# Optimization experiments

Measured on AMD Instinct MI355X. Metric: run time of the kernel, lower is better.

Reference implementation:

```python
import jax, jax.numpy as jnp
import numpy as np


def gcn_conv(x, W, b, src, dst):
    """PyG-style GCNConv: linear transform, then D^{-1/2}(A+I)D^{-1/2} aggregation."""
    N = x.shape[0]
    h = x @ W  # [N, out]
    # degree with self-loops: in-degree at target + 1
    deg = jax.ops.segment_sum(jnp.ones(src.shape[0], h.dtype), dst, num_segments=N) + 1.0
    dinv = jax.lax.rsqrt(deg)  # deg >= 1, always finite
    norm = dinv[src] * dinv[dst]  # [E]
    agg = jax.ops.segment_sum(h[src] * norm[:, None], dst, num_segments=N)
    # self-loop contribution: norm_ii = dinv_i^2
    agg = agg + h * (dinv * dinv)[:, None]
    return agg + b


def setup_inputs() -> dict:
    key = jax.random.key(0)
    ks = jax.random.split(key, 5)
    N, E, D = 50000, 800000, 512
    x = jax.random.normal(ks[0], (N, D), dtype=jnp.float32)
    edge_index = jax.random.randint(ks[1], (2, E), 0, N, dtype=jnp.int64)
    def glorot(k, fan_in, fan_out):
        s = jnp.sqrt(6.0 / (fan_in + fan_out)).astype(jnp.float32)
        return jax.random.uniform(k, (fan_in, fan_out), jnp.float32, -s, s)
    return {
        "x": x,
        "edge_index": edge_index,
        "W1": glorot(ks[2], 512, 128), "b1": jnp.zeros((128,), jnp.float32),
        "W2": glorot(ks[3], 128, 64), "b2": jnp.zeros((64,), jnp.float32),
        "W3": glorot(ks[4], 64, 64), "b3": jnp.zeros((64,), jnp.float32),
    }


def reference(x, edge_index, W1, b1, W2, b2, W3, b3):
    src, dst = edge_index[0], edge_index[1]
    h = gcn_conv(x, W1, b1, src, dst)
    h = jax.nn.leaky_relu(h, negative_slope=0.2)
    # dropout p=0.3 is identity in eval mode
    h = gcn_conv(h, W2, b2, src, dst)
    h = jax.nn.leaky_relu(h, negative_slope=0.2)
    h = gcn_conv(h, W3, b3, src, dst)
    return h
```

## Files before the change

kernel.cpp:

```cpp
#include <hip/hip_runtime.h>
#include <hip/hip_fp16.h>


typedef __attribute__((ext_vector_type(8))) short bf16x8;
typedef __attribute__((ext_vector_type(8))) _Float16 f16x8;
typedef __attribute__((ext_vector_type(4))) float f32x4;
typedef unsigned short u16;
typedef unsigned int u32;

static inline size_t alignup(size_t v, size_t a) { return (v + a - 1) & ~(a - 1); }

__device__ __forceinline__ u32 pack_hi16(u32 b0, u32 b1) {
    return __builtin_amdgcn_perm(b1, b0, 0x07060302u);
}

__device__ __forceinline__ void splitW_bf16(const float* __restrict__ W,
                                            u16* __restrict__ Wh,
                                            u16* __restrict__ Wl, int s, int F) {
    int c = s % F;
    int kb = (s / F) * 8;
    union { u32 u[4]; bf16x8 v; } hi, lo;
#pragma unroll
    for (int p = 0; p < 4; p++) {
        float x0 = W[(size_t)(kb + 2 * p) * F + c];
        float x1 = W[(size_t)(kb + 2 * p + 1) * F + c];
        u32 b0 = __float_as_uint(x0), b1 = __float_as_uint(x1);
        float l0 = x0 - __uint_as_float(b0 & 0xFFFF0000u);
        float l1 = x1 - __uint_as_float(b1 & 0xFFFF0000u);
        hi.u[p] = pack_hi16(b0, b1);
        lo.u[p] = pack_hi16(__float_as_uint(l0), __float_as_uint(l1));
    }
    *(bf16x8*)(Wh + (size_t)s * 8) = hi.v;
    *(bf16x8*)(Wl + (size_t)s * 8) = lo.v;
}

__device__ __forceinline__ void splitW_f16(const float* __restrict__ W,
                                           u16* __restrict__ Wh,
                                           u16* __restrict__ Wl, int s, int F) {
    int c = s % F;
    int kb = (s / F) * 8;
    union { u16 u[8]; bf16x8 v; } hi, lo;
#pragma unroll
    for (int p = 0; p < 8; p++) {
        float xv = W[(size_t)(kb + p) * F + c];
        __half h = __float2half(xv);
        __half l = __float2half(xv - __half2float(h));
        hi.u[p] = __half_as_ushort(h);
        lo.u[p] = __half_as_ushort(l);
    }
    *(bf16x8*)(Wh + (size_t)s * 8) = hi.v;
    *(bf16x8*)(Wl + (size_t)s * 8) = lo.v;
}

__global__ void k_init_deg(const int* __restrict__ ei, int E,
                           int* __restrict__ flag,
                           int* __restrict__ deg, int* __restrict__ rank,
                           const float* __restrict__ W1, u16* w1h, u16* w1l,
                           const float* __restrict__ W2, u16* w2h, u16* w2l,
                           const float* __restrict__ W3, u16* w3h, u16* w3l) {
    constexpr int SPLITB = 38;
    int b = blockIdx.x;
    if (b < SPLITB) {
        if (b == 0 && threadIdx.x < 64) {
            int v = ei[2 * threadIdx.x + 1];
            unsigned long long m = __ballot(v != 0);
            if (threadIdx.x == 0) *flag = (m == 0ull) ? 1 : 0;
        }
        int s = b * 256 + threadIdx.x;
        if (s < 8192) splitW_bf16(W1, w1h, w1l, s, 128);
        else if (s < 9216) splitW_f16(W2, w2h, w2l, s - 8192, 64);
        else if (s < 9728) splitW_f16(W3, w3h, w3l, s - 9216, 64);
        return;
    }
    int v = ei[2 * (threadIdx.x & 63) + 1];
    unsigned long long m = __ballot(v != 0);
    int is64 = (m == 0ull) ? 1 : 0;
    int i = (b - SPLITB) * 256 + threadIdx.x;
    if (i >= E) return;
    int d = is64 ? ei[2 * (E + i)] : ei[E + i];
    rank[i] = atomicAdd(&deg[d], 1);
}

__global__ void k_scan1(const int* __restrict__ deg, int* __restrict__ offs,
                        int* __restrict__ bsums, float* __restrict__ dinv, int N) {
    __shared__ int s[256];
    int i = blockIdx.x * 256 + threadIdx.x;
    int v = (i < N) ? deg[i] : 0;
    if (i < N) dinv[i] = rsqrtf((float)v + 1.0f);
    s[threadIdx.x] = v;
    __syncthreads();
    for (int off = 1; off < 256; off <<= 1) {
        int t = (threadIdx.x >= off) ? s[threadIdx.x - off] : 0;
        __syncthreads();
        s[threadIdx.x] += t;
        __syncthreads();
    }
    if (i < N) offs[i] = s[threadIdx.x] - v;
    if (threadIdx.x == 255) bsums[blockIdx.x] = s[255];
}

__global__ void k_scan23(int* __restrict__ offs, const int* __restrict__ bsums,
                         int nb, int N, int E) {
    __shared__ int s[256];
    int tid = threadIdx.x;
    s[tid] = (tid < nb) ? bsums[tid] : 0;
    __syncthreads();
    for (int off = 1; off < 256; off <<= 1) {
        int t = (tid >= off) ? s[tid - off] : 0;
        __syncthreads();
        s[tid] += t;
        __syncthreads();
    }
    int boff = (blockIdx.x > 0) ? s[blockIdx.x - 1] : 0;
    int i = blockIdx.x * 256 + tid;
    if (i < N) offs[i] += boff;
    if (i == 0) offs[N] = E;
}

__global__ __launch_bounds__(128) void k_gemm1_fill(
        const float* __restrict__ X,
        const u16* __restrict__ Wh, const u16* __restrict__ Wl,
        const float* __restrict__ dinv, __half* __restrict__ Hh, int N,
        int rowtiles,
        const int* __restrict__ ei, int E, const int* __restrict__ flag,
        const int* __restrict__ offs, const int* __restrict__ rank,
        int* __restrict__ csr) {
    constexpr int K = 512, F = 128, MF = 4, NF = 4, NT = K / 32;
    __shared__ float4 smemA[2][512];

    if ((int)blockIdx.x >= rowtiles) {
        int i = ((int)blockIdx.x - rowtiles) * 128 + threadIdx.x;
        if (i < E) {
            int is64 = *flag;
            int s = is64 ? ei[2 * i] : ei[i];
            int d = is64 ? ei[2 * (E + i)] : ei[E + i];
            csr[offs[d] + rank[i]] = s;
        }
        return;
    }

    const int tid = threadIdx.x;
    const int lane = tid & 63;
    const int w = tid >> 6;
    const int colbase = w * (NF * 16);
    const int lg = lane >> 4, li = lane & 15;
    const int row0 = blockIdx.x * 64;

    auto stage = [&](int b, int t) {
#pragma unroll
        for (int j = 0; j < 4; j++) {
            int c_lin = j * 128 + tid;
            int row = c_lin >> 3, c = c_lin & 7;
            int rg = row0 + row;
            if (rg >= N) rg = N - 1;
            int cs = c ^ (row & 7);
            const float* g = X + (size_t)rg * K + t * 32 + cs * 4;
            char* l = (char*)&smemA[b][0] + j * 2048 + w * 1024;
            __builtin_amdgcn_global_load_lds(
                (const __attribute__((address_space(1))) void*)g,
                (__attribute__((address_space(3))) void*)l, 16, 0, 0);
        }
    };

    f32x4 acc[MF][NF];
#pragma unroll
    for (int m = 0; m < MF; m++)
#pragma unroll
        for (int n = 0; n < NF; n++) acc[m][n] = (f32x4){0.f, 0.f, 0.f, 0.f};

    stage(0, 0);
    __syncthreads();

    for (int t = 0; t < NT; t++) {
        const int b = t & 1;
        bf16x8 bh[NF], bl[NF];
        size_t slot0 = (size_t)(t * 4 + lg) * F + colbase + li;
#pragma unroll
        for (int n = 0; n < NF; n++) {
            bh[n] = *(const bf16x8*)(Wh + (slot0 + n * 16) * 8);
            bl[n] = *(const bf16x8*)(Wl + (slot0 + n * 16) * 8);
        }
        __builtin_amdgcn_sched_barrier(0);
        if (t + 1 < NT) stage(b ^ 1, t + 1);
        const float4* lt = &smemA[b][0];
        bf16x8 ah[MF], al[MF];
#pragma unroll
        for (int m = 0; m < MF; m++) {
            int row = m * 16 + li;
            int base = row * 8, sw = row & 7;
            float4 c0 = lt[base + ((2 * lg) ^ sw)];
            float4 c1 = lt[base + ((2 * lg + 1) ^ sw)];
            float xv[8] = {c0.x, c0.y, c0.z, c0.w, c1.x, c1.y, c1.z, c1.w};
            union { u32 u[4]; bf16x8 v; } hi, lo;
#pragma unroll
            for (int q = 0; q < 4; q++) {
                u32 b0 = __float_as_uint(xv[2 * q]);
                u32 b1 = __float_as_uint(xv[2 * q + 1]);
                float l0 = xv[2 * q]     - __uint_as_float(b0 & 0xFFFF0000u);
                float l1 = xv[2 * q + 1] - __uint_as_float(b1 & 0xFFFF0000u);
                hi.u[q] = pack_hi16(b0, b1);
                lo.u[q] = pack_hi16(__float_as_uint(l0), __float_as_uint(l1));
            }
            ah[m] = hi.v;
            al[m] = lo.v;
        }
#pragma unroll
        for (int m = 0; m < MF; m++)
#pragma unroll
            for (int n = 0; n < NF; n++) {
                acc[m][n] = __builtin_amdgcn_mfma_f32_16x16x32_bf16(ah[m], bh[n], acc[m][n], 0, 0, 0);
                acc[m][n] = __builtin_amdgcn_mfma_f32_16x16x32_bf16(ah[m], bl[n], acc[m][n], 0, 0, 0);
                acc[m][n] = __builtin_amdgcn_mfma_f32_16x16x32_bf16(al[m], bh[n], acc[m][n], 0, 0, 0);
            }
        __syncthreads();
    }

#pragma unroll
    for (int m = 0; m < MF; m++) {
        int rb = row0 + m * 16 + lg * 4;
#pragma unroll
        for (int r = 0; r < 4; r++) {
            int gr = rb + r;
            if (gr >= N) continue;
            float di = dinv[gr];
#pragma unroll
            for (int n = 0; n < NF; n++) {
                int col = colbase + n * 16 + li;
                Hh[(size_t)gr * F + col] = __float2half(acc[m][n][r] * di);
            }
        }
    }
}

template <int K>
__device__ __forceinline__ void gemm_f16_body(
        const __half* __restrict__ Y,
        const u16* __restrict__ Wh, const u16* __restrict__ Wl,
        const float* __restrict__ dinv, __half* __restrict__ Hh, int N) {
    constexpr int F = 64, MF = 4, NF = 2, NT = K / 32;
    __shared__ float4 smemA[2][256];

    const int tid = threadIdx.x;
    const int lane = tid & 63;
    const int w = tid >> 6;
    const int colbase = w * (NF * 16);
    const int lg = lane >> 4, li = lane & 15;
    const int row0 = blockIdx.x * 64;

    auto stage = [&](int b, int t) {
#pragma unroll
        for (int j = 0; j < 2; j++) {
            int c_lin = j * 128 + tid;
            int row = c_lin >> 2, c = c_lin & 3;
            int rg = row0 + row;
            if (rg >= N) rg = N - 1;
            int cs = c ^ (row & 3);
            const __half* g = Y + (size_t)rg * K + t * 32 + cs * 8;
            char* l = (char*)&smemA[b][0] + j * 2048 + w * 1024;
            __builtin_amdgcn_global_load_lds(
                (const __attribute__((address_space(1))) void*)g,
                (__attribute__((address_space(3))) void*)l, 16, 0, 0);
        }
    };

    f32x4 acc[MF][NF];
#pragma unroll
    for (int m = 0; m < MF; m++)
#pragma unroll
        for (int n = 0; n < NF; n++) acc[m][n] = (f32x4){0.f, 0.f, 0.f, 0.f};

    stage(0, 0);
    __syncthreads();

    for (int t = 0; t < NT; t++) {
        const int b = t & 1;
        f16x8 bh[NF], bl[NF];
        size_t slot0 = (size_t)(t * 4 + lg) * F + colbase + li;
#pragma unroll
        for (int n = 0; n < NF; n++) {
            bh[n] = *(const f16x8*)(Wh + (slot0 + n * 16) * 8);
            bl[n] = *(const f16x8*)(Wl + (slot0 + n * 16) * 8);
        }
        __builtin_amdgcn_sched_barrier(0);
        if (t + 1 < NT) stage(b ^ 1, t + 1);
        const float4* lt = &smemA[b][0];
        f16x8 a[MF];
#pragma unroll
        for (int m = 0; m < MF; m++) {
            int row = m * 16 + li;
            union { float4 f; f16x8 h; } u;
            u.f = lt[row * 4 + (lg ^ (row & 3))];
            a[m] = u.h;
        }
#pragma unroll
        for (int m = 0; m < MF; m++)
#pragma unroll
            for (int n = 0; n < NF; n++) {
                acc[m][n] = __builtin_amdgcn_mfma_f32_16x16x32_f16(a[m], bh[n], acc[m][n], 0, 0, 0);
                acc[m][n] = __builtin_amdgcn_mfma_f32_16x16x32_f16(a[m], bl[n], acc[m][n], 0, 0, 0);
            }
        __syncthreads();
    }

#pragma unroll
    for (int m = 0; m < MF; m++) {
        int rb = row0 + m * 16 + lg * 4;
#pragma unroll
        for (int r = 0; r < 4; r++) {
            int gr = rb + r;
            if (gr >= N) continue;
            float di = dinv[gr];
#pragma unroll
            for (int n = 0; n < NF; n++) {
                int col = colbase + n * 16 + li;
                Hh[(size_t)gr * F + col] = __float2half(acc[m][n][r] * di);
            }
        }
    }
}

__global__ __launch_bounds__(128) void k_gemm2(
        const __half* __restrict__ Y, const u16* __restrict__ Wh,
        const u16* __restrict__ Wl, const float* __restrict__ dinv,
        __half* __restrict__ Hh, int N) {
    gemm_f16_body<128>(Y, Wh, Wl, dinv, Hh, N);
}
__global__ __launch_bounds__(128) void k_gemm3(
        const __half* __restrict__ Y, const u16* __restrict__ Wh,
        const u16* __restrict__ Wl, const float* __restrict__ dinv,
        __half* __restrict__ Hh, int N) {
    gemm_f16_body<64>(Y, Wh, Wl, dinv, Hh, N);
}

__global__ __launch_bounds__(256) void k_agg128(const __half* __restrict__ Hh,
                                                const int* __restrict__ offs,
                                                const int* __restrict__ csr,
                                                const float* __restrict__ dinv,
                                                const float* __restrict__ bias,
                                                __half* __restrict__ Y, int N) {
    int node = blockIdx.x * 4 + (threadIdx.x >> 6);
    int lane = threadIdx.x & 63;
    if (node >= N) return;
    const __half2* H2 = (const __half2*)Hh;
    float ax = 0.f, ay = 0.f;
    int o0 = offs[node], o1 = offs[node + 1];
    int e = o0;
    for (; e + 8 <= o1; e += 8) {
        int s[8];
#pragma unroll
        for (int q = 0; q < 8; q++) s[q] = csr[e + q];
        float2 f[8];
#pragma unroll
        for (int q = 0; q < 8; q++)
            f[q] = __half22float2(H2[(size_t)s[q] * 64 + lane]);
#pragma unroll
        for (int q = 0; q < 8; q++) { ax += f[q].x; ay += f[q].y; }
    }
    for (; e + 4 <= o1; e += 4) {
        int s0 = csr[e], s1 = csr[e + 1], s2 = csr[e + 2], s3 = csr[e + 3];
        float2 f0 = __half22float2(H2[(size_t)s0 * 64 + lane]);
        float2 f1 = __half22float2(H2[(size_t)s1 * 64 + lane]);
        float2 f2 = __half22float2(H2[(size_t)s2 * 64 + lane]);
        float2 f3 = __half22float2(H2[(size_t)s3 * 64 + lane]);
        ax += (f0.x + f1.x) + (f2.x + f3.x);
        ay += (f0.y + f1.y) + (f2.y + f3.y);
    }
    for (; e < o1; ++e) {
        float2 f0 = __half22float2(H2[(size_t)csr[e] * 64 + lane]);
        ax += f0.x; ay += f0.y;
    }
    float2 fs = __half22float2(H2[(size_t)node * 64 + lane]);
    float di = dinv[node];
    float2 bv = ((const float2*)bias)[lane];
    float vx = di * (ax + fs.x) + bv.x;
    float vy = di * (ay + fs.y) + bv.y;
    vx = vx > 0.f ? vx : 0.2f * vx;
    vy = vy > 0.f ? vy : 0.2f * vy;
    ((__half2*)Y)[(size_t)node * 64 + lane] = __floats2half2_rn(vx, vy);
}

template <bool RELU, bool OUT16>
__device__ __forceinline__ void agg64_body(const __half* __restrict__ Hh,
                                           const int* __restrict__ offs,
                                           const int* __restrict__ csr,
                                           const float* __restrict__ dinv,
                                           const float* __restrict__ bias,
                                           void* __restrict__ Y, int N) {
    int node = blockIdx.x * 8 + (threadIdx.x >> 5);
    int lane = threadIdx.x & 31;
    if (node >= N) return;
    const __half2* H2 = (const __half2*)Hh;
    float ax = 0.f, ay = 0.f;
    int o0 = offs[node], o1 = offs[node + 1];
    int e = o0;
    for (; e + 8 <= o1; e += 8) {
        int s[8];
#pragma unroll
        for (int q = 0; q < 8; q++) s[q] = csr[e + q];
        float2 f[8];
#pragma unroll
        for (int q = 0; q < 8; q++)
            f[q] = __half22float2(H2[(size_t)s[q] * 32 + lane]);
#pragma unroll
        for (int q = 0; q < 8; q++) { ax += f[q].x; ay += f[q].y; }
    }
    for (; e + 4 <= o1; e += 4) {
        int s0 = csr[e], s1 = csr[e + 1], s2 = csr[e + 2], s3 = csr[e + 3];
        float2 f0 = __half22float2(H2[(size_t)s0 * 32 + lane]);
        float2 f1 = __half22float2(H2[(size_t)s1 * 32 + lane]);
        float2 f2 = __half22float2(H2[(size_t)s2 * 32 + lane]);
        float2 f3 = __half22float2(H2[(size_t)s3 * 32 + lane]);
        ax += (f0.x + f1.x) + (f2.x + f3.x);
        ay += (f0.y + f1.y) + (f2.y + f3.y);
    }
    for (; e < o1; ++e) {
        float2 f0 = __half22float2(H2[(size_t)csr[e] * 32 + lane]);
        ax += f0.x; ay += f0.y;
    }
    float2 fs = __half22float2(H2[(size_t)node * 32 + lane]);
    float di = dinv[node];
    float2 bv = ((const float2*)bias)[lane];
    float vx = di * (ax + fs.x) + bv.x;
    float vy = di * (ay + fs.y) + bv.y;
    if (RELU) { vx = vx > 0.f ? vx : 0.2f * vx; vy = vy > 0.f ? vy : 0.2f * vy; }
    if (OUT16)
        ((__half2*)Y)[(size_t)node * 32 + lane] = __floats2half2_rn(vx, vy);
    else
        ((float2*)Y)[(size_t)node * 32 + lane] = make_float2(vx, vy);
}

__global__ __launch_bounds__(256) void k_agg64y(const __half* Hh, const int* offs,
                                                const int* csr, const float* dinv,
                                                const float* bias, __half* Y, int N) {
    agg64_body<true, true>(Hh, offs, csr, dinv, bias, Y, N);
}
__global__ __launch_bounds__(256) void k_agg64out(const __half* Hh, const int* offs,
                                                  const int* csr, const float* dinv,
                                                  const float* bias, float* Y, int N) {
    agg64_body<false, false>(Hh, offs, csr, dinv, bias, Y, N);
}

extern "C" void kernel_launch(void* const* d_in, const int* in_sizes, int n_in,
                              void* d_out, int out_size, void* d_ws, size_t ws_size,
                              hipStream_t stream) {
    const float* x  = (const float*)d_in[0];
    const int*   ei = (const int*)d_in[1];
    const float* W1 = (const float*)d_in[2];
    const float* b1 = (const float*)d_in[3];
    const float* W2 = (const float*)d_in[4];
    const float* b2 = (const float*)d_in[5];
    const float* W3 = (const float*)d_in[6];
    const float* b3 = (const float*)d_in[7];

    const int N = in_sizes[0] / 512;
    const int E = in_sizes[1] / 2;
    const int nb = (N + 255) / 256;

    char* w = (char*)d_ws;
    auto take = [&](size_t bytes) -> char* {
        char* p = w;
        w += alignup(bytes, 256);
        return p;
    };
    int*    flag  = (int*)take(256);
    int*    deg   = (int*)take((size_t)N * 4);
    int*    offs  = (int*)take((size_t)(N + 1) * 4);
    int*    bsums = (int*)take((size_t)nb * 4);
    int*    csr   = (int*)take((size_t)E * 4);
    int*    rank  = (int*)take((size_t)E * 4);
    float*  dinv  = (float*)take((size_t)N * 4);
    __half* bufA  = (__half*)take((size_t)N * 128 * 2);
    __half* bufY  = (__half*)take((size_t)N * 128 * 2);
    u16*    w1h   = (u16*)take((size_t)512 * 128 * 2);
    u16*    w1l   = (u16*)take((size_t)512 * 128 * 2);
    u16*    w2h   = (u16*)take((size_t)128 * 64 * 2);
    u16*    w2l   = (u16*)take((size_t)128 * 64 * 2);
    u16*    w3h   = (u16*)take((size_t)64 * 64 * 2);
    u16*    w3l   = (u16*)take((size_t)64 * 64 * 2);

    const int TB = 256;
    hipMemsetAsync(deg, 0, (size_t)N * 4, stream);
    const int degb = (E + TB - 1) / TB;
    k_init_deg<<<38 + degb, TB, 0, stream>>>(ei, E, flag, deg, rank,
                                             W1, w1h, w1l, W2, w2h, w2l,
                                             W3, w3h, w3l);
    k_scan1<<<nb, 256, 0, stream>>>(deg, offs, bsums, dinv, N);
    k_scan23<<<nb, 256, 0, stream>>>(offs, bsums, nb, N, E);

    const int rowtiles = (N + 63) / 64;
    const int fillblocks = (E + 127) / 128;
    k_gemm1_fill<<<rowtiles + fillblocks, 128, 0, stream>>>(
        x, w1h, w1l, dinv, bufA, N, rowtiles, ei, E, flag, offs, rank, csr);
    k_agg128<<<(N + 3) / 4, 256, 0, stream>>>(bufA, offs, csr, dinv, b1, bufY, N);
    k_gemm2<<<rowtiles, 128, 0, stream>>>(bufY, w2h, w2l, dinv, bufA, N);
    k_agg64y<<<(N + 7) / 8, 256, 0, stream>>>(bufA, offs, csr, dinv, b2, bufY, N);
    k_gemm3<<<rowtiles, 128, 0, stream>>>(bufY, w3h, w3l, dinv, bufA, N);
    k_agg64out<<<(N + 7) / 8, 256, 0, stream>>>(bufA, offs, csr, dinv, b3,
                                                (float*)d_out, N);
}
```

Baseline: 182.0 us.

## Fuse layer aggregation with following GEMM through a shared-memory tile

The layer-1 and layer-2 aggregation kernels now keep each 32-node block's activated output in a swizzled LDS tile. The same block then runs the next layer's split-precision MFMA GEMM from that tile, replacing separate aggregate and GEMM kernels. This drops two launches and the global write and re-read of the intermediate activations. In exchange each block handles fewer rows, loses the double-buffered staging, and the gather phase loops over 8 nodes per wave serially, which may lower gather parallelism.

Result: no change. 181.7 us (-0.2%).

```diff
diff --git a/kernel.cpp b/kernel.cpp
--- a/kernel.cpp
+++ b/kernel.cpp
@@ -232,160 +232,203 @@
     }
 }
 
-template <int K>
-__device__ __forceinline__ void gemm_f16_body(
-        const __half* __restrict__ Y,
+__global__ __launch_bounds__(256) void k_agg1_gemm2(
+        const __half* __restrict__ Hh, const int* __restrict__ offs,
+        const int* __restrict__ csr, const float* __restrict__ dinv,
+        const float* __restrict__ bias,
         const u16* __restrict__ Wh, const u16* __restrict__ Wl,
-        const float* __restrict__ dinv, __half* __restrict__ Hh, int N) {
-    constexpr int F = 64, MF = 4, NF = 2, NT = K / 32;
-    __shared__ float4 smemA[2][256];
+        __half* __restrict__ Out, int N) {
+    __shared__ float4 ytile[512];
+    __half2* yh2 = (__half2*)ytile;
 
     const int tid = threadIdx.x;
     const int lane = tid & 63;
     const int w = tid >> 6;
-    const int colbase = w * (NF * 16);
+    const int node0 = blockIdx.x * 32;
+    const __half2* H2 = (const __half2*)Hh;
+
+#pragma unroll 1
+    for (int q = 0; q < 8; q++) {
+        int r = w * 8 + q;
+        int node = node0 + r;
+        if (node < N) {
+            float ax = 0.f, ay = 0.f;
+            int o0 = offs[node], o1 = offs[node + 1];
+            int e = o0;
+            for (; e + 8 <= o1; e += 8) {
+                int s[8];
+#pragma unroll
+                for (int p = 0; p < 8; p++) s[p] = csr[e + p];
+                float2 f[8];
+#pragma unroll
+                for (int p = 0; p < 8; p++)
+                    f[p] = __half22float2(H2[(size_t)s[p] * 64 + lane]);
+#pragma unroll
+                for (int p = 0; p < 8; p++) { ax += f[p].x; ay += f[p].y; }
+            }
+            for (; e < o1; ++e) {
+                float2 f0 = __half22float2(H2[(size_t)csr[e] * 64 + lane]);
+                ax += f0.x; ay += f0.y;
+            }
+            float2 fs = __half22float2(H2[(size_t)node * 64 + lane]);
+            float di = dinv[node];
+            float2 bv = ((const float2*)bias)[lane];
+            float vx = di * (ax + fs.x) + bv.x;
+            float vy = di * (ay + fs.y) + bv.y;
+            vx = vx > 0.f ? vx : 0.2f * vx;
+            vy = vy > 0.f ? vy : 0.2f * vy;
+            int c = lane >> 2, pos = lane & 3;
+            int cc = c ^ (r & 15);
+            yh2[r * 64 + cc * 4 + pos] = __floats2half2_rn(vx, vy);
+        }
+    }
+    __syncthreads();
+
+    constexpr int NF = 2, NT = 4, F = 64;
+    const int wr = (w >> 1) * 16;
+    const int wc = (w & 1) * 32;
     const int lg = lane >> 4, li = lane & 15;
-    const int row0 = blockIdx.x * 64;
-
-    auto stage = [&](int b, int t) {
-#pragma unroll
-        for (int j = 0; j < 2; j++) {
-            int c_lin = j * 128 + tid;
-            int row = c_lin >> 2, c = c_lin & 3;
-            int rg = row0 + row;
-            if (rg >= N) rg = N - 1;
-            int cs = c ^ (row & 3);
-            const __half* g = Y + (size_t)rg * K + t * 32 + cs * 8;
-            char* l = (char*)&smemA[b][0] + j * 2048 + w * 1024;
-            __builtin_amdgcn_global_load_lds(
-                (const __attribute__((address_space(1))) void*)g,
-                (__attribute__((address_space(3))) void*)l, 16, 0, 0);
-        }
-    };
-
-    f32x4 acc[MF][NF];
-#pragma unroll
-    for (int m = 0; m < MF; m++)
-#pragma unroll
-        for (int n = 0; n < NF; n++) acc[m][n] = (f32x4){0.f, 0.f, 0.f, 0.f};
-
-    stage(0, 0);
-    __syncthreads();
-
+
+    f32x4 acc[NF];
+#pragma unroll
+    for (int n = 0; n < NF; n++) acc[n] = (f32x4){0.f, 0.f, 0.f, 0.f};
+
+#pragma unroll
     for (int t = 0; t < NT; t++) {
-        const int b = t & 1;
         f16x8 bh[NF], bl[NF];
-        size_t slot0 = (size_t)(t * 4 + lg) * F + colbase + li;
+        size_t slot0 = (size_t)(t * 4 + lg) * F + wc + li;
 #pragma unroll
         for (int n = 0; n < NF; n++) {
             bh[n] = *(const f16x8*)(Wh + (slot0 + n * 16) * 8);
             bl[n] = *(const f16x8*)(Wl + (slot0 + n * 16) * 8);
         }
-        __builtin_amdgcn_sched_barrier(0);
-        if (t + 1 < NT) stage(b ^ 1, t + 1);
-        const float4* lt = &smemA[b][0];
-        f16x8 a[MF];
-#pragma unroll
-        for (int m = 0; m < MF; m++) {
-            int row = m * 16 + li;
-            union { float4 f; f16x8 h; } u;
-            u.f = lt[row * 4 + (lg ^ (row & 3))];
-            a[m] = u.h;
-        }
-#pragma unroll
-        for (int m = 0; m < MF; m++)
-#pragma unroll
-            for (int n = 0; n < NF; n++) {
-                acc[m][n] = __builtin_amdgcn_mfma_f32_16x16x32_f16(a[m], bh[n], acc[m][n], 0, 0, 0);
-                acc[m][n] = __builtin_amdgcn_mfma_f32_16x16x32_f16(a[m], bl[n], acc[m][n], 0, 0, 0);
-            }
-        __syncthreads();
-    }
-
-#pragma unroll
-    for (int m = 0; m < MF; m++) {
-        int rb = row0 + m * 16 + lg * 4;
-#pragma unroll
-        for (int r = 0; r < 4; r++) {
-            int gr = rb + r;
-            if (gr >= N) continue;
-            float di = dinv[gr];
-#pragma unroll
-            for (int n = 0; n < NF; n++) {
-                int col = colbase + n * 16 + li;
-                Hh[(size_t)gr * F + col] = __float2half(acc[m][n][r] * di);
-            }
-        }
-    }
-}
-
-__global__ __launch_bounds__(128) void k_gemm2(
-        const __half* __restrict__ Y, const u16* __restrict__ Wh,
-        const u16* __restrict__ Wl, const float* __restrict__ dinv,
-        __half* __restrict__ Hh, int N) {
-    gemm_f16_body<128>(Y, Wh, Wl, dinv, Hh, N);
-}
-__global__ __launch_bounds__(128) void k_gemm3(
-        const __half* __restrict__ Y, const u16* __restrict__ Wh,
-        const u16* __restrict__ Wl, const float* __restrict__ dinv,
-        __half* __restrict__ Hh, int N) {
-    gemm_f16_body<64>(Y, Wh, Wl, dinv, Hh, N);
-}
-
-__global__ __launch_bounds__(256) void k_agg128(const __half* __restrict__ Hh,
-                                                const int* __restrict__ offs,
-                                                const int* __restrict__ csr,
-                                                const float* __restrict__ dinv,
-                                                const float* __restrict__ bias,
-                                                __half* __restrict__ Y, int N) {
-    int node = blockIdx.x * 4 + (threadIdx.x >> 6);
-    int lane = threadIdx.x & 63;
-    if (node >= N) return;
+        int r = wr + li;
+        int c = t * 4 + lg;
+        union { float4 f; f16x8 h; } u;
+        u.f = ytile[r * 16 + (c ^ li)];
+        f16x8 a = u.h;
+#pragma unroll
+        for (int n = 0; n < NF; n++) {
+            acc[n] = __builtin_amdgcn_mfma_f32_16x16x32_f16(a, bh[n], acc[n], 0, 0, 0);
+            acc[n] = __builtin_amdgcn_mfma_f32_16x16x32_f16(a, bl[n], acc[n], 0, 0, 0);
+        }
+    }
+
+#pragma unroll
+    for (int rr = 0; rr < 4; rr++) {
+        int gr = node0 + wr + lg * 4 + rr;
+        if (gr >= N) continue;
+        float di = dinv[gr];
+#pragma unroll
+        for (int n = 0; n < NF; n++) {
+            int col = wc + n * 16 + li;
+            Out[(size_t)gr * F + col] = __float2half(acc[n][rr] * di);
+        }
+    }
+}
+
+__global__ __launch_bounds__(256) void k_agg2_gemm3(
+        const __half* __restrict__ Hh, const int* __restrict__ offs,
+        const int* __restrict__ csr, const float* __restrict__ dinv,
+        const float* __restrict__ bias,
+        const u16* __restrict__ Wh, const u16* __restrict__ Wl,
+        __half* __restrict__ Out, int N) {
+    __shared__ float4 ytile[256];
+    __half2* yh2 = (__half2*)ytile;
+
+    const int tid = threadIdx.x;
+    const int lane = tid & 63;
+    const int w = tid >> 6;
+    const int node0 = blockIdx.x * 32;
     const __half2* H2 = (const __half2*)Hh;
-    float ax = 0.f, ay = 0.f;
-    int o0 = offs[node], o1 = offs[node + 1];
-    int e = o0;
-    for (; e + 8 <= o1; e += 8) {
-        int s[8];
-#pragma unroll
-        for (int q = 0; q < 8; q++) s[q] = csr[e + q];
-        float2 f[8];
-#pragma unroll
-        for (int q = 0; q < 8; q++)
-            f[q] = __half22float2(H2[(size_t)s[q] * 64 + lane]);
-#pragma unroll
-        for (int q = 0; q < 8; q++) { ax += f[q].x; ay += f[q].y; }
-    }
-    for (; e + 4 <= o1; e += 4) {
-        int s0 = csr[e], s1 = csr[e + 1], s2 = csr[e + 2], s3 = csr[e + 3];
-        float2 f0 = __half22float2(H2[(size_t)s0 * 64 + lane]);
-        float2 f1 = __half22float2(H2[(size_t)s1 * 64 + lane]);
-        float2 f2 = __half22float2(H2[(size_t)s2 * 64 + lane]);
-        float2 f3 = __half22float2(H2[(size_t)s3 * 64 + lane]);
-        ax += (f0.x + f1.x) + (f2.x + f3.x);
-        ay += (f0.y + f1.y) + (f2.y + f3.y);
-    }
-    for (; e < o1; ++e) {
-        float2 f0 = __half22float2(H2[(size_t)csr[e] * 64 + lane]);
-        ax += f0.x; ay += f0.y;
-    }
-    float2 fs = __half22float2(H2[(size_t)node * 64 + lane]);
-    float di = dinv[node];
-    float2 bv = ((const float2*)bias)[lane];
-    float vx = di * (ax + fs.x) + bv.x;
-    float vy = di * (ay + fs.y) + bv.y;
-    vx = vx > 0.f ? vx : 0.2f * vx;
-    vy = vy > 0.f ? vy : 0.2f * vy;
-    ((__half2*)Y)[(size_t)node * 64 + lane] = __floats2half2_rn(vx, vy);
-}
-
-template <bool RELU, bool OUT16>
-__device__ __forceinline__ void agg64_body(const __half* __restrict__ Hh,
-                                           const int* __restrict__ offs,
-                                           const int* __restrict__ csr,
-                                           const float* __restrict__ dinv,
-                                           const float* __restrict__ bias,
-                                           void* __restrict__ Y, int N) {
+
+#pragma unroll 1
+    for (int q = 0; q < 4; q++) {
+        int r = w * 8 + q * 2 + (lane >> 5);
+        int node = node0 + r;
+        int l = lane & 31;
+        if (node < N) {
+            float ax = 0.f, ay = 0.f;
+            int o0 = offs[node], o1 = offs[node + 1];
+            int e = o0;
+            for (; e + 8 <= o1; e += 8) {
+                int s[8];
+#pragma unroll
+                for (int p = 0; p < 8; p++) s[p] = csr[e + p];
+                float2 f[8];
+#pragma unroll
+                for (int p = 0; p < 8; p++)
+                    f[p] = __half22float2(H2[(size_t)s[p] * 32 + l]);
+#pragma unroll
+                for (int p = 0; p < 8; p++) { ax += f[p].x; ay += f[p].y; }
+            }
+            for (; e < o1; ++e) {
+                float2 f0 = __half22float2(H2[(size_t)csr[e] * 32 + l]);
+                ax += f0.x; ay += f0.y;
+            }
+            float2 fs = __half22float2(H2[(size_t)node * 32 + l]);
+            float di = dinv[node];
+            float2 bv = ((const float2*)bias)[l];
+            float vx = di * (ax + fs.x) + bv.x;
+            float vy = di * (ay + fs.y) + bv.y;
+            vx = vx > 0.f ? vx : 0.2f * vx;
+            vy = vy > 0.f ? vy : 0.2f * vy;
+            int c = l >> 2, pos = l & 3;
+            int cc = c ^ (r & 7);
+            yh2[r * 32 + cc * 4 + pos] = __floats2half2_rn(vx, vy);
+        }
+    }
+    __syncthreads();
+
+    constexpr int NF = 2, NT = 2, F = 64;
+    const int wr = (w >> 1) * 16;
+    const int wc = (w & 1) * 32;
+    const int lg = lane >> 4, li = lane & 15;
+
+    f32x4 acc[NF];
+#pragma unroll
+    for (int n = 0; n < NF; n++) acc[n] = (f32x4){0.f, 0.f, 0.f, 0.f};
+
+#pragma unroll
+    for (int t = 0; t < NT; t++) {
+        f16x8 bh[NF], bl[NF];
+        size_t slot0 = (size_t)(t * 4 + lg) * F + wc + li;
+#pragma unroll
+        for (int n = 0; n < NF; n++) {
+            bh[n] = *(const f16x8*)(Wh + (slot0 + n * 16) * 8);
+            bl[n] = *(const f16x8*)(Wl + (slot0 + n * 16) * 8);
+        }
+        int r = wr + li;
+        int c = t * 4 + lg;
+        union { float4 f; f16x8 h; } u;
+        u.f = ytile[r * 8 + (c ^ (li & 7))];
+        f16x8 a = u.h;
+#pragma unroll
+        for (int n = 0; n < NF; n++) {
+            acc[n] = __builtin_amdgcn_mfma_f32_16x16x32_f16(a, bh[n], acc[n], 0, 0, 0);
+            acc[n] = __builtin_amdgcn_mfma_f32_16x16x32_f16(a, bl[n], acc[n], 0, 0, 0);
+        }
+    }
+
+#pragma unroll
+    for (int rr = 0; rr < 4; rr++) {
+        int gr = node0 + wr + lg * 4 + rr;
+        if (gr >= N) continue;
+        float di = dinv[gr];
+#pragma unroll
+        for (int n = 0; n < NF; n++) {
+            int col = wc + n * 16 + li;
+            Out[(size_t)gr * F + col] = __float2half(acc[n][rr] * di);
+        }
+    }
+}
+
+__global__ __launch_bounds__(256) void k_agg64out(const __half* __restrict__ Hh,
+                                                  const int* __restrict__ offs,
+                                                  const int* __restrict__ csr,
+                                                  const float* __restrict__ dinv,
+                                                  const float* __restrict__ bias,
+                                                  float* __restrict__ Y, int N) {
     int node = blockIdx.x * 8 + (threadIdx.x >> 5);
     int lane = threadIdx.x & 31;
     if (node >= N) return;
@@ -422,22 +465,7 @@
     float2 bv = ((const float2*)bias)[lane];
     float vx = di * (ax + fs.x) + bv.x;
     float vy = di * (ay + fs.y) + bv.y;
-    if (RELU) { vx = vx > 0.f ? vx : 0.2f * vx; vy = vy > 0.f ? vy : 0.2f * vy; }
-    if (OUT16)
-        ((__half2*)Y)[(size_t)node * 32 + lane] = __floats2half2_rn(vx, vy);
-    else
-        ((float2*)Y)[(size_t)node * 32 + lane] = make_float2(vx, vy);
-}
-
-__global__ __launch_bounds__(256) void k_agg64y(const __half* Hh, const int* offs,
-                                                const int* csr, const float* dinv,
-                                                const float* bias, __half* Y, int N) {
-    agg64_body<true, true>(Hh, offs, csr, dinv, bias, Y, N);
-}
-__global__ __launch_bounds__(256) void k_agg64out(const __half* Hh, const int* offs,
-                                                  const int* csr, const float* dinv,
-                                                  const float* bias, float* Y, int N) {
-    agg64_body<false, false>(Hh, offs, csr, dinv, bias, Y, N);
+    ((float2*)Y)[(size_t)node * 32 + lane] = make_float2(vx, vy);
 }
 
 extern "C" void kernel_launch(void* const* d_in, const int* in_sizes, int n_in,
@@ -470,7 +498,7 @@
     int*    rank  = (int*)take((size_t)E * 4);
     float*  dinv  = (float*)take((size_t)N * 4);
     __half* bufA  = (__half*)take((size_t)N * 128 * 2);
-    __half* bufY  = (__half*)take((size_t)N * 128 * 2);
+    __half* bufB  = (__half*)take((size_t)N * 128 * 2);
     u16*    w1h   = (u16*)take((size_t)512 * 128 * 2);
     u16*    w1l   = (u16*)take((size_t)512 * 128 * 2);
     u16*    w2h   = (u16*)take((size_t)128 * 64 * 2);
@@ -489,12 +517,13 @@
 
     const int rowtiles = (N + 63) / 64;
     const int fillblocks = (E + 127) / 128;
+    const int fuseblocks = (N + 31) / 32;
     k_gemm1_fill<<<rowtiles + fillblocks, 128, 0, stream>>>(
         x, w1h, w1l, dinv, bufA, N, rowtiles, ei, E, flag, offs, rank, csr);
-    k_agg128<<<(N + 3) / 4, 256, 0, stream>>>(bufA, offs, csr, dinv, b1, bufY, N);
-    k_gemm2<<<rowtiles, 128, 0, stream>>>(bufY, w2h, w2l, dinv, bufA, N);
-    k_agg64y<<<(N + 7) / 8, 256, 0, stream>>>(bufA, offs, csr, dinv, b2, bufY, N);
-    k_gemm3<<<rowtiles, 128, 0, stream>>>(bufY, w3h, w3l, dinv, bufA, N);
+    k_agg1_gemm2<<<fuseblocks, 256, 0, stream>>>(bufA, offs, csr, dinv, b1,
+                                                 w2h, w2l, bufB, N);
+    k_agg2_gemm3<<<fuseblocks, 256, 0, stream>>>(bufB, offs, csr, dinv, b2,
+                                                 w3h, w3l, bufA, N);
     k_agg64out<<<(N + 7) / 8, 256, 0, stream>>>(bufA, offs, csr, dinv, b3,
                                                 (float*)d_out, N);
 }
```
